# Kernel tuning notes

Hardware: AMD Instinct MI355X
Metric: run time of the kernel (lower is better)

## Reference

```python
import jax, jax.numpy as jnp
import numpy as np

N_NODES = 60000
IN_CH = 128
HID = 32
ACT_DIM = 6
N_EDGES = 600000


def setup_inputs() -> dict:
    key = jax.random.key(0)
    ks = jax.random.split(key, 10)
    state = jax.random.normal(ks[0], (N_NODES, IN_CH), dtype=jnp.float32)
    edge_index = jax.random.randint(ks[1], (2, N_EDGES), 0, N_NODES, dtype=jnp.int64)
    s_g = 1.0 / np.sqrt(IN_CH)
    s_h = 1.0 / np.sqrt(HID)
    Wg = jax.random.uniform(ks[2], (IN_CH, IN_CH), jnp.float32, -s_g, s_g)
    bg = jax.random.uniform(ks[3], (IN_CH,), jnp.float32, -s_g, s_g)
    W1 = jax.random.uniform(ks[4], (IN_CH, HID), jnp.float32, -s_g, s_g)
    b1 = jax.random.uniform(ks[5], (HID,), jnp.float32, -s_g, s_g)
    W2 = jax.random.uniform(ks[6], (HID, HID), jnp.float32, -s_h, s_h)
    b2 = jax.random.uniform(ks[7], (HID,), jnp.float32, -s_h, s_h)
    W3 = jax.random.uniform(ks[8], (HID, 1), jnp.float32, -s_h, s_h)
    b3 = jax.random.uniform(ks[9], (1,), jnp.float32, -s_h, s_h)
    return {"state": state, "Wg": Wg, "bg": bg, "W1": W1, "b1": b1,
            "W2": W2, "b2": b2, "W3": W3, "b3": b3, "edge_index": edge_index}


def reference(state, Wg, bg, W1, b1, W2, b2, W3, b3, edge_index):
    N = state.shape[0]
    # GCNConv: add self-loops, symmetric degree normalization
    loop = jnp.arange(N, dtype=edge_index.dtype)
    src = jnp.concatenate([edge_index[0], loop])
    dst = jnp.concatenate([edge_index[1], loop])
    deg = jax.ops.segment_sum(jnp.ones_like(dst, dtype=state.dtype), dst, num_segments=N)
    dinv = jax.lax.rsqrt(deg)  # deg >= 1 thanks to self-loops
    norm = dinv[src] * dinv[dst]  # [E+N]
    h = state @ Wg  # [N, C]
    agg = jax.ops.segment_sum(h[src] * norm[:, None], dst, num_segments=N) + bg
    out = jax.nn.relu(agg)
    x = (out + state).reshape(-1, ACT_DIM, IN_CH)  # [B, 6, C]
    x = jax.nn.leaky_relu(x @ W1 + b1)
    x = jax.nn.leaky_relu(x @ W2 + b2)
    conc = jax.nn.softplus(x @ W3 + b3)[..., 0]  # [B, 6]
    # deterministic, mode==0
    action = conc / (conc.sum() + 1e-20)
    return action
```

## Files before the change

kernel.cpp:

```cpp
#include <hip/hip_runtime.h>
#include <hip/hip_bf16.h>
#include <math.h>

#define N_NODES 60000
#define IN_CH   128
#define HID     32
#define N_EDGES 600000
#define CAP     32

#define WS_CNT    0
#define WS_SUM    60000
#define WS_BUCKET 60008
#define WS_HS     2940032
#define WS_X      10620032

typedef float  v4f __attribute__((ext_vector_type(4)));
typedef short  v8s __attribute__((ext_vector_type(8)));

static __device__ inline short f2bf(float f) {
    __hip_bfloat16 h = __float2bfloat16(f);
    union { __hip_bfloat16 h; short s; } u; u.h = h; return u.s;
}
static __device__ inline float bflo(unsigned int u) { return __uint_as_float(u << 16); }
static __device__ inline float bfhi(unsigned int u) { return __uint_as_float(u & 0xffff0000u); }
static __device__ inline int   rdl_i(int v, int l)   { return __builtin_amdgcn_readlane(v, l); }
static __device__ inline float rdl_f(float v, int l) {
    return __int_as_float(__builtin_amdgcn_readlane(__float_as_int(v), l));
}

__launch_bounds__(256)
__global__ void k_fat(const float* __restrict__ state, const float* __restrict__ Wg,
                      const int* __restrict__ eidx, int* __restrict__ cnt,
                      int* __restrict__ bucket, unsigned short* __restrict__ hs) {
    __shared__ __align__(16) short Bs[128 * 136];
    const int bid = blockIdx.x;
    const int r7 = bid % 7, q7 = bid / 7;
    const int t = threadIdx.x;

    if (r7 >= 2) {
        const int hb = q7 * 5 + (r7 - 2);
        const int i = hb * 256 + t;
        if (i < N_EDGES) {
            int s = eidx[i];
            int d = eidx[N_EDGES + i];
            int slot = atomicAdd(&cnt[d], 1);
            if (slot < CAP) bucket[d * CAP + slot] = s;
        }
        return;
    }

    const int gb = q7 * 2 + r7;

    for (int idx = t; idx < 128 * 128; idx += 256) {
        int k = idx >> 7, n = idx & 127;
        Bs[n * 136 + k] = f2bf(Wg[idx]);
    }
    __syncthreads();

    const int w = t >> 6, lane = t & 63;
    const int quad = lane >> 4, m = lane & 15;
    const int rowBase = gb * 64;
    int arow = rowBase + w * 16 + m;
    if (arow > N_NODES - 1) arow = N_NODES - 1;

    v8s a[4];
    const float4* sp = (const float4*)(state + (size_t)arow * 128);
#pragma unroll
    for (int q = 0; q < 4; ++q) {
        float4 v0 = sp[q * 8 + quad * 2];
        float4 v1 = sp[q * 8 + quad * 2 + 1];
        v8s af;
        af[0] = f2bf(v0.x); af[1] = f2bf(v0.y); af[2] = f2bf(v0.z); af[3] = f2bf(v0.w);
        af[4] = f2bf(v1.x); af[5] = f2bf(v1.y); af[6] = f2bf(v1.z); af[7] = f2bf(v1.w);
        a[q] = af;
    }

    v4f acc[8];
#pragma unroll
    for (int tt = 0; tt < 8; ++tt) acc[tt] = (v4f)0.f;

#pragma unroll
    for (int tt = 0; tt < 8; ++tt) {
        const short* bp = &Bs[(tt * 16 + m) * 136];
#pragma unroll
        for (int q = 0; q < 4; ++q) {
            v8s b = *(const v8s*)(bp + q * 32 + quad * 8);
            acc[tt] = __builtin_amdgcn_mfma_f32_16x16x32_bf16(a[q], b, acc[tt], 0, 0, 0);
        }
    }

#pragma unroll
    for (int tt = 0; tt < 8; ++tt) {
#pragma unroll
        for (int r = 0; r < 4; ++r) {
            int rr = rowBase + w * 16 + quad * 4 + r;
            if (rr < N_NODES)
                hs[(size_t)rr * 128 + tt * 16 + m] = (unsigned short)f2bf(acc[tt][r]);
        }
    }
}

__launch_bounds__(256)
__global__ void k_gather(const unsigned short* __restrict__ hs, const float* __restrict__ state,
                         const int* __restrict__ cnt, const int* __restrict__ bucket,
                         const float* __restrict__ bg, unsigned int* __restrict__ xb) {
    const int wave = threadIdx.x >> 6, lane = threadIdx.x & 63;
    const int row = blockIdx.x * 4 + wave;
    if (row >= N_NODES) return;
    const int ci = cnt[row];
    const float dinv = rsqrtf((float)ci + 1.0f);
    const int nb = ci < CAP ? ci : CAP;

    int slot = 0; float dv = 0.f;
    if (lane < nb) {
        slot = bucket[row * CAP + lane];
        dv = rsqrtf((float)cnt[slot] + 1.0f);
    }

    const unsigned int* hp = (const unsigned int*)hs;
    float ax, ay;
    {
        unsigned int u = hp[(unsigned)row * 64u + lane];
        ax = bflo(u) * dinv;
        ay = bfhi(u) * dinv;
    }
    int s = 0;
    for (; s + 8 <= nb; s += 8) {
        int   s0 = rdl_i(slot, s + 0), s1 = rdl_i(slot, s + 1);
        int   s2 = rdl_i(slot, s + 2), s3 = rdl_i(slot, s + 3);
        int   s4 = rdl_i(slot, s + 4), s5 = rdl_i(slot, s + 5);
        int   s6 = rdl_i(slot, s + 6), s7 = rdl_i(slot, s + 7);
        float d0 = rdl_f(dv, s + 0), d1 = rdl_f(dv, s + 1);
        float d2 = rdl_f(dv, s + 2), d3 = rdl_f(dv, s + 3);
        float d4 = rdl_f(dv, s + 4), d5 = rdl_f(dv, s + 5);
        float d6 = rdl_f(dv, s + 6), d7 = rdl_f(dv, s + 7);
        unsigned int u0 = hp[(unsigned)s0 * 64u + lane];
        unsigned int u1 = hp[(unsigned)s1 * 64u + lane];
        unsigned int u2 = hp[(unsigned)s2 * 64u + lane];
        unsigned int u3 = hp[(unsigned)s3 * 64u + lane];
        unsigned int u4 = hp[(unsigned)s4 * 64u + lane];
        unsigned int u5 = hp[(unsigned)s5 * 64u + lane];
        unsigned int u6 = hp[(unsigned)s6 * 64u + lane];
        unsigned int u7 = hp[(unsigned)s7 * 64u + lane];
        ax = fmaf(d0, bflo(u0), ax); ay = fmaf(d0, bfhi(u0), ay);
        ax = fmaf(d1, bflo(u1), ax); ay = fmaf(d1, bfhi(u1), ay);
        ax = fmaf(d2, bflo(u2), ax); ay = fmaf(d2, bfhi(u2), ay);
        ax = fmaf(d3, bflo(u3), ax); ay = fmaf(d3, bfhi(u3), ay);
        ax = fmaf(d4, bflo(u4), ax); ay = fmaf(d4, bfhi(u4), ay);
        ax = fmaf(d5, bflo(u5), ax); ay = fmaf(d5, bfhi(u5), ay);
        ax = fmaf(d6, bflo(u6), ax); ay = fmaf(d6, bfhi(u6), ay);
        ax = fmaf(d7, bflo(u7), ax); ay = fmaf(d7, bfhi(u7), ay);
    }
    for (; s + 4 <= nb; s += 4) {
        int   s0 = rdl_i(slot, s + 0), s1 = rdl_i(slot, s + 1);
        int   s2 = rdl_i(slot, s + 2), s3 = rdl_i(slot, s + 3);
        float d0 = rdl_f(dv, s + 0), d1 = rdl_f(dv, s + 1);
        float d2 = rdl_f(dv, s + 2), d3 = rdl_f(dv, s + 3);
        unsigned int u0 = hp[(unsigned)s0 * 64u + lane];
        unsigned int u1 = hp[(unsigned)s1 * 64u + lane];
        unsigned int u2 = hp[(unsigned)s2 * 64u + lane];
        unsigned int u3 = hp[(unsigned)s3 * 64u + lane];
        ax = fmaf(d0, bflo(u0), ax); ay = fmaf(d0, bfhi(u0), ay);
        ax = fmaf(d1, bflo(u1), ax); ay = fmaf(d1, bfhi(u1), ay);
        ax = fmaf(d2, bflo(u2), ax); ay = fmaf(d2, bfhi(u2), ay);
        ax = fmaf(d3, bflo(u3), ax); ay = fmaf(d3, bfhi(u3), ay);
    }
    for (; s < nb; ++s) {
        int   s0 = rdl_i(slot, s);
        float d0 = rdl_f(dv, s);
        unsigned int u = hp[(unsigned)s0 * 64u + lane];
        ax = fmaf(d0, bflo(u), ax);
        ay = fmaf(d0, bfhi(u), ay);
    }
    float2 bgv = ((const float2*)bg)[lane];
    float2 st  = ((const float2*)state)[(unsigned)row * 64u + lane];
    float ox = fmaxf(fmaf(dinv, ax, bgv.x), 0.f) + st.x;
    float oy = fmaxf(fmaf(dinv, ay, bgv.y), 0.f) + st.y;
    unsigned int pack = ((unsigned int)(unsigned short)f2bf(oy) << 16)
                      | ((unsigned int)(unsigned short)f2bf(ox));
    xb[(unsigned)row * 64u + lane] = pack;
}

__launch_bounds__(256)
__global__ void k_mlp(const unsigned int* __restrict__ xb,
                      const float* __restrict__ W1, const float* __restrict__ b1,
                      const float* __restrict__ W2, const float* __restrict__ b2,
                      const float* __restrict__ W3, const float* __restrict__ b3,
                      float* __restrict__ out, float* __restrict__ sum) {
    __shared__ float4 W1s[128 * 8];
    __shared__ float4 W2s[32 * 8];
    __shared__ float  W3s[32];
    __shared__ float  wred[4];
    const int t = threadIdx.x;
#pragma unroll
    for (int i = 0; i < 4; ++i) W1s[t + 256 * i] = ((const float4*)W1)[t + 256 * i];
    W2s[t] = ((const float4*)W2)[t];
    if (t < 32) W3s[t] = W3[t];
    __syncthreads();

    const int r = blockIdx.x * 256 + t;
    float sp = 0.f;
    if (r < N_NODES) {
        float h1[32];
#pragma unroll
        for (int j = 0; j < 32; ++j) h1[j] = b1[j];
        const v8s* xr = (const v8s*)(xb + (size_t)r * 64);
#pragma unroll 2
        for (int k8 = 0; k8 < 16; ++k8) {
            v8s xv = xr[k8];
#pragma unroll
            for (int jj = 0; jj < 8; ++jj) {
                float xk = __uint_as_float(((unsigned int)(unsigned short)xv[jj]) << 16);
                const int k = k8 * 8 + jj;
#pragma unroll
                for (int j4 = 0; j4 < 8; ++j4) {
                    float4 w = W1s[k * 8 + j4];
                    h1[j4 * 4 + 0] = fmaf(xk, w.x, h1[j4 * 4 + 0]);
                    h1[j4 * 4 + 1] = fmaf(xk, w.y, h1[j4 * 4 + 1]);
                    h1[j4 * 4 + 2] = fmaf(xk, w.z, h1[j4 * 4 + 2]);
                    h1[j4 * 4 + 3] = fmaf(xk, w.w, h1[j4 * 4 + 3]);
                }
            }
        }
        float z1[32];
#pragma unroll
        for (int j = 0; j < 32; ++j) z1[j] = h1[j] > 0.f ? h1[j] : 0.01f * h1[j];
        float h2[32];
#pragma unroll
        for (int j = 0; j < 32; ++j) h2[j] = b2[j];
#pragma unroll
        for (int k = 0; k < 32; ++k) {
            float zk = z1[k];
#pragma unroll
            for (int j4 = 0; j4 < 8; ++j4) {
                float4 w = W2s[k * 8 + j4];
                h2[j4 * 4 + 0] = fmaf(zk, w.x, h2[j4 * 4 + 0]);
                h2[j4 * 4 + 1] = fmaf(zk, w.y, h2[j4 * 4 + 1]);
                h2[j4 * 4 + 2] = fmaf(zk, w.z, h2[j4 * 4 + 2]);
                h2[j4 * 4 + 3] = fmaf(zk, w.w, h2[j4 * 4 + 3]);
            }
        }
        float a3 = b3[0];
#pragma unroll
        for (int j = 0; j < 32; ++j) {
            float z2 = h2[j] > 0.f ? h2[j] : 0.01f * h2[j];
            a3 = fmaf(z2, W3s[j], a3);
        }
        sp = fmaxf(a3, 0.f) + log1pf(expf(-fabsf(a3)));
        out[r] = sp;
    }
    float p = sp;
#pragma unroll
    for (int off = 32; off >= 1; off >>= 1) p += __shfl_xor(p, off, 64);
    if ((t & 63) == 0) wred[t >> 6] = p;
    __syncthreads();
    if (t == 0) atomicAdd(sum, (wred[0] + wred[1]) + (wred[2] + wred[3]));
}

__global__ void k_norm(const float* __restrict__ sum, float* __restrict__ out) {
    int i = blockIdx.x * blockDim.x + threadIdx.x;
    if (i < N_NODES / 4) {
        float inv = 1.0f / (*sum + 1e-20f);
        float4* o4 = (float4*)out;
        float4 v = o4[i];
        v.x *= inv; v.y *= inv; v.z *= inv; v.w *= inv;
        o4[i] = v;
    }
}

extern "C" void kernel_launch(void* const* d_in, const int* in_sizes, int n_in,
                              void* d_out, int out_size, void* d_ws, size_t ws_size,
                              hipStream_t stream) {
    const float* state = (const float*)d_in[0];
    const float* Wg    = (const float*)d_in[1];
    const float* bg    = (const float*)d_in[2];
    const float* W1    = (const float*)d_in[3];
    const float* b1    = (const float*)d_in[4];
    const float* W2    = (const float*)d_in[5];
    const float* b2    = (const float*)d_in[6];
    const float* W3    = (const float*)d_in[7];
    const float* b3    = (const float*)d_in[8];
    const int*   eidx  = (const int*)d_in[9];
    float* out = (float*)d_out;

    int*   wi = (int*)d_ws;
    float* wf = (float*)d_ws;
    int*   cnt    = wi + WS_CNT;
    float* sum    = wf + WS_SUM;
    int*   bucket = wi + WS_BUCKET;
    unsigned short* hs = (unsigned short*)(wf + WS_HS);
    unsigned int*   xb = (unsigned int*)(wf + WS_X);

    hipMemsetAsync(cnt, 0, 60001 * sizeof(int), stream);

    k_fat<<<3282, 256, 0, stream>>>(state, Wg, eidx, cnt, bucket, hs);
    k_gather<<<(N_NODES + 3) / 4, 256, 0, stream>>>(hs, state, cnt, bucket, bg, xb);
    k_mlp<<<(N_NODES + 255) / 256, 256, 0, stream>>>(xb, W1, b1, W2, b2, W3, b3, out, sum);
    k_norm<<<(N_NODES / 4 + 255) / 256, 256, 0, stream>>>(sum, out);
}
```

Measured before the change: 178.9 us.

## Compute first MLP layer with bf16 MFMA using split hi/lo weights

Replaces the scalar per-thread 128x32 FMA loop in the MLP kernel with MFMA 16x16x32 bf16 instructions. Each wave now handles 16 rows, and W1 is split into high and low bf16 parts so the product keeps near-fp32 weight precision. The second layer is spread across lane quads through a shared-memory staging buffer, and the final dot product is reduced with shuffles. The goal is to remove the heavy LDS and VALU cost of the old per-row loop. In exchange it doubles the MFMA count and adds shared-memory traffic.

Measured after the change: 177.4 us. Within noise of the previous version (-0.9%).

```diff
diff --git a/kernel.cpp b/kernel.cpp
--- a/kernel.cpp
+++ b/kernel.cpp
@@ -20,6 +20,9 @@
 static __device__ inline short f2bf(float f) {
     __hip_bfloat16 h = __float2bfloat16(f);
     union { __hip_bfloat16 h; short s; } u; u.h = h; return u.s;
+}
+static __device__ inline float bf2f(short s) {
+    return __uint_as_float(((unsigned int)(unsigned short)s) << 16);
 }
 static __device__ inline float bflo(unsigned int u) { return __uint_as_float(u << 16); }
 static __device__ inline float bfhi(unsigned int u) { return __uint_as_float(u & 0xffff0000u); }
@@ -187,72 +190,94 @@
                       const float* __restrict__ W2, const float* __restrict__ b2,
                       const float* __restrict__ W3, const float* __restrict__ b3,
                       float* __restrict__ out, float* __restrict__ sum) {
-    __shared__ float4 W1s[128 * 8];
+    __shared__ __align__(16) short BsH[32 * 136];
+    __shared__ __align__(16) short BsL[32 * 136];
+    __shared__ float  zs[4][16 * 33];
     __shared__ float4 W2s[32 * 8];
-    __shared__ float  W3s[32];
+    __shared__ float  b1s[32], b2s[32], W3s[32];
     __shared__ float  wred[4];
     const int t = threadIdx.x;
-#pragma unroll
-    for (int i = 0; i < 4; ++i) W1s[t + 256 * i] = ((const float4*)W1)[t + 256 * i];
+
+    for (int idx = t; idx < 128 * 32; idx += 256) {
+        int k = idx >> 5, j = idx & 31;
+        float f = W1[idx];
+        short hi = f2bf(f);
+        short lo = f2bf(f - bf2f(hi));
+        BsH[j * 136 + k] = hi;
+        BsL[j * 136 + k] = lo;
+    }
     W2s[t] = ((const float4*)W2)[t];
-    if (t < 32) W3s[t] = W3[t];
+    if (t < 32) { b1s[t] = b1[t]; b2s[t] = b2[t]; W3s[t] = W3[t]; }
     __syncthreads();
 
-    const int r = blockIdx.x * 256 + t;
-    float sp = 0.f;
-    if (r < N_NODES) {
-        float h1[32];
-#pragma unroll
-        for (int j = 0; j < 32; ++j) h1[j] = b1[j];
-        const v8s* xr = (const v8s*)(xb + (size_t)r * 64);
-#pragma unroll 2
-        for (int k8 = 0; k8 < 16; ++k8) {
-            v8s xv = xr[k8];
-#pragma unroll
-            for (int jj = 0; jj < 8; ++jj) {
-                float xk = __uint_as_float(((unsigned int)(unsigned short)xv[jj]) << 16);
-                const int k = k8 * 8 + jj;
-#pragma unroll
-                for (int j4 = 0; j4 < 8; ++j4) {
-                    float4 w = W1s[k * 8 + j4];
-                    h1[j4 * 4 + 0] = fmaf(xk, w.x, h1[j4 * 4 + 0]);
-                    h1[j4 * 4 + 1] = fmaf(xk, w.y, h1[j4 * 4 + 1]);
-                    h1[j4 * 4 + 2] = fmaf(xk, w.z, h1[j4 * 4 + 2]);
-                    h1[j4 * 4 + 3] = fmaf(xk, w.w, h1[j4 * 4 + 3]);
-                }
-            }
-        }
-        float z1[32];
-#pragma unroll
-        for (int j = 0; j < 32; ++j) z1[j] = h1[j] > 0.f ? h1[j] : 0.01f * h1[j];
-        float h2[32];
-#pragma unroll
-        for (int j = 0; j < 32; ++j) h2[j] = b2[j];
+    const int wv = t >> 6, lane = t & 63;
+    const int quad = lane >> 4, m = lane & 15;
+    const int rbase = (blockIdx.x * 4 + wv) * 16;
+    float wavesum = 0.f;
+
+    if (rbase < N_NODES) {
+        v8s a[4];
+        const int4* xp = (const int4*)(xb + (size_t)(rbase + m) * 64);
+#pragma unroll
+        for (int q = 0; q < 4; ++q) a[q] = *(const v8s*)&xp[q * 4 + quad];
+
+        v4f acc0 = (v4f)0.f, acc1 = (v4f)0.f;
+#pragma unroll
+        for (int q = 0; q < 4; ++q) {
+            v8s bh0 = *(const v8s*)&BsH[m * 136 + q * 32 + quad * 8];
+            v8s bh1 = *(const v8s*)&BsH[(16 + m) * 136 + q * 32 + quad * 8];
+            acc0 = __builtin_amdgcn_mfma_f32_16x16x32_bf16(a[q], bh0, acc0, 0, 0, 0);
+            acc1 = __builtin_amdgcn_mfma_f32_16x16x32_bf16(a[q], bh1, acc1, 0, 0, 0);
+        }
+#pragma unroll
+        for (int q = 0; q < 4; ++q) {
+            v8s bl0 = *(const v8s*)&BsL[m * 136 + q * 32 + quad * 8];
+            v8s bl1 = *(const v8s*)&BsL[(16 + m) * 136 + q * 32 + quad * 8];
+            acc0 = __builtin_amdgcn_mfma_f32_16x16x32_bf16(a[q], bl0, acc0, 0, 0, 0);
+            acc1 = __builtin_amdgcn_mfma_f32_16x16x32_bf16(a[q], bl1, acc1, 0, 0, 0);
+        }
+
+        float bj0 = b1s[m], bj1 = b1s[16 + m];
+#pragma unroll
+        for (int r = 0; r < 4; ++r) {
+            float h0 = acc0[r] + bj0; h0 = h0 > 0.f ? h0 : 0.01f * h0;
+            float h1 = acc1[r] + bj1; h1 = h1 > 0.f ? h1 : 0.01f * h1;
+            zs[wv][(quad * 4 + r) * 33 + m]      = h0;
+            zs[wv][(quad * 4 + r) * 33 + 16 + m] = h1;
+        }
+        asm volatile("s_waitcnt lgkmcnt(0)" ::: "memory");
+
+        float h2[8];
+#pragma unroll
+        for (int j = 0; j < 8; ++j) h2[j] = b2s[quad * 8 + j];
+        const float* zrow = &zs[wv][m * 33];
 #pragma unroll
         for (int k = 0; k < 32; ++k) {
-            float zk = z1[k];
-#pragma unroll
-            for (int j4 = 0; j4 < 8; ++j4) {
-                float4 w = W2s[k * 8 + j4];
-                h2[j4 * 4 + 0] = fmaf(zk, w.x, h2[j4 * 4 + 0]);
-                h2[j4 * 4 + 1] = fmaf(zk, w.y, h2[j4 * 4 + 1]);
-                h2[j4 * 4 + 2] = fmaf(zk, w.z, h2[j4 * 4 + 2]);
-                h2[j4 * 4 + 3] = fmaf(zk, w.w, h2[j4 * 4 + 3]);
-            }
-        }
-        float a3 = b3[0];
-#pragma unroll
-        for (int j = 0; j < 32; ++j) {
+            float zk = zrow[k];
+            float4 wA = W2s[k * 8 + quad * 2];
+            float4 wB = W2s[k * 8 + quad * 2 + 1];
+            h2[0] = fmaf(zk, wA.x, h2[0]); h2[1] = fmaf(zk, wA.y, h2[1]);
+            h2[2] = fmaf(zk, wA.z, h2[2]); h2[3] = fmaf(zk, wA.w, h2[3]);
+            h2[4] = fmaf(zk, wB.x, h2[4]); h2[5] = fmaf(zk, wB.y, h2[5]);
+            h2[6] = fmaf(zk, wB.z, h2[6]); h2[7] = fmaf(zk, wB.w, h2[7]);
+        }
+        float a3p = 0.f;
+#pragma unroll
+        for (int j = 0; j < 8; ++j) {
             float z2 = h2[j] > 0.f ? h2[j] : 0.01f * h2[j];
-            a3 = fmaf(z2, W3s[j], a3);
-        }
-        sp = fmaxf(a3, 0.f) + log1pf(expf(-fabsf(a3)));
-        out[r] = sp;
-    }
-    float p = sp;
-#pragma unroll
-    for (int off = 32; off >= 1; off >>= 1) p += __shfl_xor(p, off, 64);
-    if ((t & 63) == 0) wred[t >> 6] = p;
+            a3p = fmaf(z2, W3s[quad * 8 + j], a3p);
+        }
+        a3p += __shfl_xor(a3p, 16, 64);
+        a3p += __shfl_xor(a3p, 32, 64);
+        float a3 = a3p + b3[0];
+        float sp = fmaxf(a3, 0.f) + log1pf(expf(-fabsf(a3)));
+        if (quad == 0) out[rbase + m] = sp;
+        float p = (quad == 0) ? sp : 0.f;
+#pragma unroll
+        for (int off = 32; off >= 1; off >>= 1) p += __shfl_xor(p, off, 64);
+        wavesum = p;
+    }
+    if (lane == 0) wred[wv] = wavesum;
     __syncthreads();
     if (t == 0) atomicAdd(sum, (wred[0] + wred[1]) + (wred[2] + wred[3]));
 }
@@ -295,6 +320,6 @@
 
     k_fat<<<3282, 256, 0, stream>>>(state, Wg, eidx, cnt, bucket, hs);
     k_gather<<<(N_NODES + 3) / 4, 256, 0, stream>>>(hs, state, cnt, bucket, bg, xb);
-    k_mlp<<<(N_NODES + 255) / 256, 256, 0, stream>>>(xb, W1, b1, W2, b2, W3, b3, out, sum);
+    k_mlp<<<938, 256, 0, stream>>>(xb, W1, b1, W2, b2, W3, b3, out, sum);
     k_norm<<<(N_NODES / 4 + 255) / 256, 256, 0, stream>>>(sum, out);
 }
```
